# Performance work log

Measured on AMD Instinct MI355X. Metric: run time of the kernel, lower is better.

## Reference

```python
import jax, jax.numpy as jnp
import numpy as np


def _chain_marginals(unary, pairwise, gamma):
    """Forward-backward logsumexp DP along the last axis.

    unary:    [B, K, R, L]      (R = non-scanned spatial axis)
    pairwise: [B, K, K, R, L-1] (dim1 = source state, dim2 = target state)
    returns marginals [B, K, R, L].
    """
    u_t = jnp.moveaxis(unary, -1, 0)      # [L, B, K, R]
    p_t = jnp.moveaxis(pairwise, -1, 0)   # [L-1, B, K, K, R]

    def fwd_step(c, xs):
        p, u = xs
        m = gamma * jax.nn.logsumexp((p + c[:, :, None, :]) / gamma, axis=1)
        new = u + m
        return new, new

    init_l = u_t[0]
    _, left = jax.lax.scan(fwd_step, init_l, (p_t, u_t[1:]))
    left = jnp.concatenate([init_l[None], left], axis=0)   # [L, B, K, R]

    def bwd_step(c, xs):
        p, u = xs
        m = gamma * jax.nn.logsumexp((p + c[:, None, :, :]) / gamma, axis=2)
        new = u + m
        return new, new

    init_r = u_t[-1]
    _, right = jax.lax.scan(bwd_step, init_r, (p_t[::-1], u_t[:-1][::-1]))
    right = jnp.concatenate([right[::-1], init_r[None]], axis=0)  # [L, B, K, R]

    marg = left + right - u_t
    return jnp.moveaxis(marg, 0, -1)


def reference(horizontal_unary, vertical_unary, horizontal_pairwise, vertical_pairwise, gamma):
    g = gamma[0]
    B, K, H, W = horizontal_unary.shape

    h_marg = _chain_marginals(horizontal_unary, horizontal_pairwise, g)
    # vertical: scan over the H axis by swapping the last two spatial axes
    v_marg = _chain_marginals(
        vertical_unary.swapaxes(-1, -2),
        vertical_pairwise.swapaxes(-1, -2),
        g,
    ).swapaxes(-1, -2)

    avg = (h_marg + v_marg) * 0.5
    h_unary_new = horizontal_unary - (h_marg - avg) / W
    v_unary_new = vertical_unary - (v_marg - avg) / H
    return (h_unary_new, v_unary_new, h_marg, v_marg)


def setup_inputs() -> dict:
    key = jax.random.key(0)
    k1, k2, k3, k4 = jax.random.split(key, 4)
    B, K, H, W = 4, 32, 128, 128
    return {
        "horizontal_unary": jax.random.normal(k1, (B, K, H, W), dtype=jnp.float32),
        "vertical_unary": jax.random.normal(k2, (B, K, H, W), dtype=jnp.float32),
        "horizontal_pairwise": jax.random.normal(k3, (B, K, K, H, W - 1), dtype=jnp.float32),
        "vertical_pairwise": jax.random.normal(k4, (B, K, K, H - 1, W), dtype=jnp.float32),
        "gamma": jnp.ones((1,), dtype=jnp.float32),
    }
```

## Files before the change

### kernel.cpp

```cpp
#include <hip/hip_runtime.h>

#define NF 2097152

__global__ __launch_bounds__(256) void dp_kernel(
    const float* __restrict__ hu, const float* __restrict__ vu,
    const float* __restrict__ hp, const float* __restrict__ vp,
    const float* __restrict__ gam,
    float* __restrict__ lh, float* __restrict__ rh,
    float* __restrict__ lv, float* __restrict__ rv)
{
    __shared__ float smem[16976];
    const float g  = gam[0];
    const float ig = 1.0f / g;
    const int tid = threadIdx.x;
    const int blk = blockIdx.x;

    if (blk < 128) {
        const int dir  = blk & 1;
        const int b    = (blk >> 1) & 3;
        const int rblk = blk >> 3;
        const int rl   = tid & 7;
        const int r    = rblk * 8 + rl;
        const int k    = tid >> 3;
        float* cb = smem;

        const int sIt  = dir ? 16256  : 520192;
        const int sFix = dir ? 520192 : 16256;
        const int pbase = b * 16646144 + k * sFix + r;
        const int ubase = (b * 32 + k) * 16384 + r;
        const float* __restrict__ p = vp;
        const float* __restrict__ u = vu;
        float* __restrict__ out = dir ? rv : lv;

        const int pos0 = dir ? 127 : 0;
        const float c0 = u[ubase + pos0 * 128];
        cb[k * 8 + rl] = c0;
        out[ubase + pos0 * 128] = c0;

        float pv[32], pn[32];
        {
            const int pp1 = dir ? 126 : 0;
            const int ib = pbase + pp1 * 128;
            #pragma unroll
            for (int j = 0; j < 32; ++j) pv[j] = p[ib + j * sIt];
        }
        float un  = u[ubase + (dir ? 126 : 1) * 128];
        float un2 = 0.0f;
        __syncthreads();

        for (int s = 1; s < 128; ++s) {
            const int pos = dir ? 127 - s : s;
            if (s < 127) {
                const int npp = dir ? 126 - s : s;
                const int ib = pbase + npp * 128;
                #pragma unroll
                for (int j = 0; j < 32; ++j) pn[j] = p[ib + j * sIt];
                un2 = u[ubase + (dir ? 126 - s : s + 1) * 128];
            }
            const float* cs = cb + (((s + 1) & 1) << 8);
            float mx = -3.4e38f;
            #pragma unroll
            for (int j = 0; j < 32; ++j) {
                const float v = pv[j] + cs[j * 8 + rl];
                pv[j] = v;
                mx = fmaxf(mx, v);
            }
            float ss = 0.0f;
            #pragma unroll
            for (int j = 0; j < 32; ++j) ss += __expf((pv[j] - mx) * ig);
            const float nv = un + mx + g * __logf(ss);
            out[ubase + pos * 128] = nv;
            cb[((s & 1) << 8) + k * 8 + rl] = nv;
            un = un2;
            #pragma unroll
            for (int j = 0; j < 32; ++j) pv[j] = pn[j];
            __syncthreads();
        }
    } else {
        const int hid = blk - 128;
        const int dir = hid & 1;
        const int b   = (hid >> 1) & 3;
        const int h   = hid >> 3;
        float (* __restrict__ pbuf)[1025] = (float(*)[1025])smem;
        float* cc  = smem + 16400;
        float* rmx = smem + 16464;
        float* rs  = smem + 16720;
        const float* __restrict__ p = hp;
        const float* __restrict__ u = hu;
        float* __restrict__ out = dir ? rh : lh;
        const int pb = b * 16646144 + h * 127;
        const int ub = b * 524288 + h * 128;
        const int pos0 = dir ? 127 : 0;
        if (tid < 32) {
            const float c0 = u[ub + tid * 16384 + pos0];
            cc[tid] = c0;
            out[ub + tid * 16384 + pos0] = c0;
        }
        const int k  = tid & 31;
        const int jq = tid >> 5;
        int sc = 0;
        for (int ci = 0; ci < 8; ++ci) {
            const int l0 = dir ? 112 - ci * 16 : ci * 16;
            const int nl = (l0 == 112) ? 15 : 16;
            __syncthreads();
            #pragma unroll 8
            for (int i = 0; i < 64; ++i) {
                const int q  = i * 256 + tid;
                const int jk = q >> 4, lo = q & 15;
                if (lo < nl) {
                    const float v = p[pb + jk * 16256 + l0 + lo];
                    const int col = dir ? (((jk & 31) << 5) | (jk >> 5)) : jk;
                    pbuf[lo][col] = v;
                }
            }
            __syncthreads();
            for (int li = 0; li < nl; ++li) {
                const int lo  = dir ? nl - 1 - li : li;
                const int pos = dir ? l0 + lo : l0 + lo + 1;
                const float* cs = cc + ((sc & 1) << 5);
                float vals[4];
                float pm = -3.4e38f;
                #pragma unroll
                for (int jj = 0; jj < 4; ++jj) {
                    const int j = jq * 4 + jj;
                    const float v = pbuf[lo][j * 32 + k] + cs[j];
                    vals[jj] = v;
                    pm = fmaxf(pm, v);
                }
                float ps = 0.0f;
                #pragma unroll
                for (int jj = 0; jj < 4; ++jj) ps += __expf((vals[jj] - pm) * ig);
                rmx[jq * 32 + k] = pm;
                rs [jq * 32 + k] = ps;
                __syncthreads();
                if (tid < 32) {
                    float mx = rmx[tid];
                    #pragma unroll
                    for (int q2 = 1; q2 < 8; ++q2) mx = fmaxf(mx, rmx[q2 * 32 + tid]);
                    float ssum = 0.0f;
                    #pragma unroll
                    for (int q2 = 0; q2 < 8; ++q2)
                        ssum += rs[q2 * 32 + tid] * __expf((rmx[q2 * 32 + tid] - mx) * ig);
                    const float m  = mx + g * __logf(ssum);
                    const float nv = u[ub + tid * 16384 + pos] + m;
                    out[ub + tid * 16384 + pos] = nv;
                    cc[(((sc + 1) & 1) << 5) + tid] = nv;
                }
                __syncthreads();
                ++sc;
            }
        }
    }
}

__global__ __launch_bounds__(256) void combine_kernel(
    const float* __restrict__ hu, const float* __restrict__ vu,
    const float* __restrict__ rh, const float* __restrict__ rv,
    float* __restrict__ o)
{
    const int i = blockIdx.x * 256 + threadIdx.x;
    const float4* hu4 = (const float4*)hu;
    const float4* vu4 = (const float4*)vu;
    const float4* lh4 = (const float4*)(o + 2 * (size_t)NF);
    const float4* lv4 = (const float4*)(o + 3 * (size_t)NF);
    const float4* rh4 = (const float4*)rh;
    const float4* rv4 = (const float4*)rv;
    float4* o0 = (float4*)o;
    float4* o1 = (float4*)(o + (size_t)NF);
    float4* o2 = (float4*)(o + 2 * (size_t)NF);
    float4* o3 = (float4*)(o + 3 * (size_t)NF);

    float4 A = hu4[i], B = vu4[i];
    float4 LH = lh4[i], RH = rh4[i], LV = lv4[i], RV = rv4[i];
    float4 HM, VM, U0, U1;
    const float scl = 1.0f / 256.0f;
    float* pa  = (float*)&A;  float* pb  = (float*)&B;
    float* plh = (float*)&LH; float* prh = (float*)&RH;
    float* plv = (float*)&LV; float* prv = (float*)&RV;
    float* phm = (float*)&HM; float* pvm = (float*)&VM;
    float* pu0 = (float*)&U0; float* pu1 = (float*)&U1;
    #pragma unroll
    for (int t = 0; t < 4; ++t) {
        const float hm = plh[t] + prh[t] - pa[t];
        const float vm = plv[t] + prv[t] - pb[t];
        phm[t] = hm;
        pvm[t] = vm;
        pu0[t] = pa[t] - (hm - vm) * scl;
        pu1[t] = pb[t] - (vm - hm) * scl;
    }
    o0[i] = U0; o1[i] = U1; o2[i] = HM; o3[i] = VM;
}

extern "C" void kernel_launch(void* const* d_in, const int* in_sizes, int n_in,
                              void* d_out, int out_size, void* d_ws, size_t ws_size,
                              hipStream_t stream) {
    const float* hu  = (const float*)d_in[0];
    const float* vu  = (const float*)d_in[1];
    const float* hp  = (const float*)d_in[2];
    const float* vp  = (const float*)d_in[3];
    const float* gam = (const float*)d_in[4];
    float* out = (float*)d_out;

    float* lh = out + 2 * (size_t)NF;
    float* lv = out + 3 * (size_t)NF;
    float* rh = (float*)d_ws;
    float* rv = rh + (size_t)NF;

    dp_kernel<<<1152, 256, 0, stream>>>(hu, vu, hp, vp, gam, lh, rh, lv, rv);
    combine_kernel<<<2048, 256, 0, stream>>>(hu, vu, rh, rv, out);
}
```

Before: 957.3 us.

## Use wavefront shuffles for horizontal reduction and triple-buffer vertical loads

Result: no change. 949.3 us (-0.8%).

```diff
diff --git a/kernel.cpp b/kernel.cpp
--- a/kernel.cpp
+++ b/kernel.cpp
@@ -9,7 +9,7 @@
     float* __restrict__ lh, float* __restrict__ rh,
     float* __restrict__ lv, float* __restrict__ rv)
 {
-    __shared__ float smem[16976];
+    alignas(16) __shared__ float smem[16512];
     const float g  = gam[0];
     const float ig = 1.0f / g;
     const int tid = threadIdx.x;
@@ -20,12 +20,12 @@
         const int b    = (blk >> 1) & 3;
         const int rblk = blk >> 3;
         const int rl   = tid & 7;
+        const int k    = tid >> 3;
         const int r    = rblk * 8 + rl;
-        const int k    = tid >> 3;
         float* cb = smem;
 
-        const int sIt  = dir ? 16256  : 520192;
-        const int sFix = dir ? 520192 : 16256;
+        const int sIt   = dir ? 16256  : 520192;
+        const int sFix  = dir ? 520192 : 16256;
         const int pbase = b * 16646144 + k * sFix + r;
         const int ubase = (b * 32 + k) * 16384 + r;
         const float* __restrict__ p = vp;
@@ -34,117 +34,131 @@
 
         const int pos0 = dir ? 127 : 0;
         const float c0 = u[ubase + pos0 * 128];
-        cb[k * 8 + rl] = c0;
+        cb[rl * 36 + k] = c0;
         out[ubase + pos0 * 128] = c0;
 
-        float pv[32], pn[32];
+        float b0[32], b1[32], b2[32];
+        float u0, u1, u2 = 0.0f;
         {
-            const int pp1 = dir ? 126 : 0;
-            const int ib = pbase + pp1 * 128;
+            const int i1 = pbase + (dir ? 126 : 0) * 128;
             #pragma unroll
-            for (int j = 0; j < 32; ++j) pv[j] = p[ib + j * sIt];
-        }
-        float un  = u[ubase + (dir ? 126 : 1) * 128];
-        float un2 = 0.0f;
+            for (int j = 0; j < 32; ++j) b0[j] = p[i1 + j * sIt];
+            u0 = u[ubase + (dir ? 126 : 1) * 128];
+            const int i2 = pbase + (dir ? 125 : 1) * 128;
+            #pragma unroll
+            for (int j = 0; j < 32; ++j) b1[j] = p[i2 + j * sIt];
+            u1 = u[ubase + (dir ? 125 : 2) * 128];
+        }
         __syncthreads();
 
-        for (int s = 1; s < 128; ++s) {
-            const int pos = dir ? 127 - s : s;
-            if (s < 127) {
-                const int npp = dir ? 126 - s : s;
-                const int ib = pbase + npp * 128;
-                #pragma unroll
-                for (int j = 0; j < 32; ++j) pn[j] = p[ib + j * sIt];
-                un2 = u[ubase + (dir ? 126 - s : s + 1) * 128];
-            }
-            const float* cs = cb + (((s + 1) & 1) << 8);
-            float mx = -3.4e38f;
-            #pragma unroll
-            for (int j = 0; j < 32; ++j) {
-                const float v = pv[j] + cs[j * 8 + rl];
-                pv[j] = v;
-                mx = fmaxf(mx, v);
-            }
-            float ss = 0.0f;
-            #pragma unroll
-            for (int j = 0; j < 32; ++j) ss += __expf((pv[j] - mx) * ig);
-            const float nv = un + mx + g * __logf(ss);
-            out[ubase + pos * 128] = nv;
-            cb[((s & 1) << 8) + k * 8 + rl] = nv;
-            un = un2;
-            #pragma unroll
-            for (int j = 0; j < 32; ++j) pv[j] = pn[j];
-            __syncthreads();
-        }
+#define VSTEP(S, CUR, UC, LD, UL)                                             \
+        if ((S) <= 127) {                                                     \
+            if ((S) + 2 <= 127) {                                             \
+                const int pc = dir ? 125 - (S) : (S) + 1;                     \
+                const int ib = pbase + pc * 128;                              \
+                _Pragma("unroll")                                             \
+                for (int j = 0; j < 32; ++j) LD[j] = p[ib + j * sIt];         \
+                UL = u[ubase + (dir ? 125 - (S) : (S) + 2) * 128];            \
+            }                                                                 \
+            {                                                                 \
+                const float* cs = cb + ((((S) + 1) & 1) * 288) + rl * 36;     \
+                float c4[32];                                                 \
+                _Pragma("unroll")                                             \
+                for (int jq = 0; jq < 8; ++jq) {                              \
+                    const float4 t = *(const float4*)(cs + jq * 4);           \
+                    c4[jq*4+0] = t.x; c4[jq*4+1] = t.y;                       \
+                    c4[jq*4+2] = t.z; c4[jq*4+3] = t.w;                       \
+                }                                                             \
+                float mx = -3.4e38f;                                          \
+                _Pragma("unroll")                                             \
+                for (int j = 0; j < 32; ++j) {                                \
+                    CUR[j] += c4[j]; mx = fmaxf(mx, CUR[j]);                  \
+                }                                                             \
+                float ss = 0.0f;                                              \
+                _Pragma("unroll")                                             \
+                for (int j = 0; j < 32; ++j) ss += __expf((CUR[j] - mx) * ig);\
+                const float nv = UC + mx + g * __logf(ss);                    \
+                out[ubase + (dir ? 127 - (S) : (S)) * 128] = nv;              \
+                cb[(((S) & 1) * 288) + rl * 36 + k] = nv;                     \
+            }                                                                 \
+            __syncthreads();                                                  \
+        }
+
+        for (int s = 1; s <= 127; s += 3) {
+            VSTEP(s,     b0, u0, b2, u2)
+            VSTEP(s + 1, b1, u1, b0, u0)
+            VSTEP(s + 2, b2, u2, b1, u1)
+        }
+#undef VSTEP
     } else {
         const int hid = blk - 128;
         const int dir = hid & 1;
         const int b   = (hid >> 1) & 3;
         const int h   = hid >> 3;
-        float (* __restrict__ pbuf)[1025] = (float(*)[1025])smem;
-        float* cc  = smem + 16400;
-        float* rmx = smem + 16464;
-        float* rs  = smem + 16720;
+        float (* __restrict__ pbuf)[1028] = (float(*)[1028])smem;
+        float* cc = smem + 16448;
         const float* __restrict__ p = hp;
         const float* __restrict__ u = hu;
         float* __restrict__ out = dir ? rh : lh;
         const int pb = b * 16646144 + h * 127;
         const int ub = b * 524288 + h * 128;
+        const int k  = tid >> 3;
+        const int jq = tid & 7;
+        const int uk = ub + k * 16384;
         const int pos0 = dir ? 127 : 0;
-        if (tid < 32) {
-            const float c0 = u[ub + tid * 16384 + pos0];
-            cc[tid] = c0;
-            out[ub + tid * 16384 + pos0] = c0;
-        }
-        const int k  = tid & 31;
-        const int jq = tid >> 5;
+        if (jq == 0) {
+            const float c0 = u[uk + pos0];
+            cc[k] = c0;
+            out[uk + pos0] = c0;
+        }
         int sc = 0;
+        float u_nxt = 0.0f;
         for (int ci = 0; ci < 8; ++ci) {
             const int l0 = dir ? 112 - ci * 16 : ci * 16;
             const int nl = (l0 == 112) ? 15 : 16;
-            __syncthreads();
             #pragma unroll 8
             for (int i = 0; i < 64; ++i) {
                 const int q  = i * 256 + tid;
                 const int jk = q >> 4, lo = q & 15;
                 if (lo < nl) {
                     const float v = p[pb + jk * 16256 + l0 + lo];
-                    const int col = dir ? (((jk & 31) << 5) | (jk >> 5)) : jk;
+                    const int col = dir ? jk : (((jk & 31) << 5) | (jk >> 5));
                     pbuf[lo][col] = v;
                 }
+            }
+            if (jq == 0) {
+                const int lo0  = dir ? nl - 1 : 0;
+                u_nxt = u[uk + (dir ? l0 + lo0 : l0 + lo0 + 1)];
             }
             __syncthreads();
             for (int li = 0; li < nl; ++li) {
                 const int lo  = dir ? nl - 1 - li : li;
                 const int pos = dir ? l0 + lo : l0 + lo + 1;
+                const float u_cur = u_nxt;
+                if (jq == 0 && li + 1 < nl) {
+                    const int lo2 = dir ? nl - 2 - li : li + 1;
+                    u_nxt = u[uk + (dir ? l0 + lo2 : l0 + lo2 + 1)];
+                }
                 const float* cs = cc + ((sc & 1) << 5);
-                float vals[4];
-                float pm = -3.4e38f;
+                const float4 pq = *(const float4*)&pbuf[lo][k * 32 + jq * 4];
+                const float4 cq = *(const float4*)(cs + jq * 4);
+                const float v0 = pq.x + cq.x, v1 = pq.y + cq.y;
+                const float v2 = pq.z + cq.z, v3 = pq.w + cq.w;
+                float m = fmaxf(fmaxf(v0, v1), fmaxf(v2, v3));
+                float s = __expf((v0 - m) * ig) + __expf((v1 - m) * ig)
+                        + __expf((v2 - m) * ig) + __expf((v3 - m) * ig);
                 #pragma unroll
-                for (int jj = 0; jj < 4; ++jj) {
-                    const int j = jq * 4 + jj;
-                    const float v = pbuf[lo][j * 32 + k] + cs[j];
-                    vals[jj] = v;
-                    pm = fmaxf(pm, v);
-                }
-                float ps = 0.0f;
-                #pragma unroll
-                for (int jj = 0; jj < 4; ++jj) ps += __expf((vals[jj] - pm) * ig);
-                rmx[jq * 32 + k] = pm;
-                rs [jq * 32 + k] = ps;
-                __syncthreads();
-                if (tid < 32) {
-                    float mx = rmx[tid];
-                    #pragma unroll
-                    for (int q2 = 1; q2 < 8; ++q2) mx = fmaxf(mx, rmx[q2 * 32 + tid]);
-                    float ssum = 0.0f;
-                    #pragma unroll
-                    for (int q2 = 0; q2 < 8; ++q2)
-                        ssum += rs[q2 * 32 + tid] * __expf((rmx[q2 * 32 + tid] - mx) * ig);
-                    const float m  = mx + g * __logf(ssum);
-                    const float nv = u[ub + tid * 16384 + pos] + m;
-                    out[ub + tid * 16384 + pos] = nv;
-                    cc[(((sc + 1) & 1) << 5) + tid] = nv;
+                for (int d = 1; d <= 4; d <<= 1) {
+                    const float mo = __shfl_xor(m, d, 64);
+                    const float so = __shfl_xor(s, d, 64);
+                    const float mn = fmaxf(m, mo);
+                    s = s * __expf((m - mn) * ig) + so * __expf((mo - mn) * ig);
+                    m = mn;
+                }
+                if (jq == 0) {
+                    const float nv = u_cur + m + g * __logf(s);
+                    out[uk + pos] = nv;
+                    cc[(((sc + 1) & 1) << 5) + k] = nv;
                 }
                 __syncthreads();
                 ++sc;
```
